# Kernel tuning notes

Measured on AMD Instinct MI355X. Metric: run time of the kernel, lower is better.

The kernel has to match this reference:

```python
import jax, jax.numpy as jnp
import numpy as np

C0, C1, C2 = 2000, 10000, 50000  # class cutoffs
D = 1024                          # input_size (hidden dim)
OUT_HEAD = C0 + 2                 # head output: shortlist + 2 cluster logits


def setup_inputs() -> dict:
    key = jax.random.key(0)
    ks = jax.random.split(key, 7)
    s = lambda fan_in: 1.0 / np.sqrt(fan_in)
    x = jax.random.normal(ks[0], (4096, D), dtype=jnp.float32)
    Wh = jax.random.normal(ks[1], (OUT_HEAD, D), dtype=jnp.float32) * s(D)
    bh = jnp.zeros((OUT_HEAD,), dtype=jnp.float32)
    # tail 0: D -> D//4**0 -> (C1-C0)
    W0a = jax.random.normal(ks[2], (D, D), dtype=jnp.float32) * s(D)
    W0b = jax.random.normal(ks[3], (C1 - C0, D), dtype=jnp.float32) * s(D)
    # tail 1: D -> D//4**1 -> (C2-C1)
    W1a = jax.random.normal(ks[4], (D // 4, D), dtype=jnp.float32) * s(D)
    W1b = jax.random.normal(ks[5], (C2 - C1, D // 4), dtype=jnp.float32) * s(D // 4)
    return {"x": x, "Wh": Wh, "bh": bh, "W0a": W0a, "W0b": W0b, "W1a": W1a, "W1b": W1b}


def reference(x, Wh, bh, W0a, W0b, W1a, W1b):
    # head: [B, OUT_HEAD]; log-softmax over shortlist + cluster logits
    lsm_head = jax.nn.log_softmax(x @ Wh.T + bh, axis=-1)
    # tail clusters: capacity-reduction linear, projection, log-softmax within cluster
    lsm_t0 = jax.nn.log_softmax((x @ W0a.T) @ W0b.T, axis=-1)  # [B, C1-C0]
    lsm_t1 = jax.nn.log_softmax((x @ W1a.T) @ W1b.T, axis=-1)  # [B, C2-C1]
    # flat log-probs: cluster log-prob broadcast-added to within-cluster log-probs
    prob = jnp.concatenate([
        lsm_head[:, :C0],
        lsm_head[:, C0:C0 + 1] + lsm_t0,
        lsm_head[:, C0 + 1:C0 + 2] + lsm_t1,
    ], axis=1)  # [B, C2]
    return prob
```

## Files before the change

kernel.cpp:

```cpp
#include <hip/hip_runtime.h>
#include <hip/hip_bf16.h>
#include <math.h>

#define CC0 2000
#define CC1 10000
#define CC2 50000
#define DH  1024
#define BATCH 4096
#define OUT_HEAD (CC0 + 2)

#define N0_P 8192
#define N1_P 40192
#define NH_P 2048

typedef __attribute__((ext_vector_type(4))) float  f32x4;
typedef __attribute__((ext_vector_type(8))) __bf16 bf16x8;
typedef __attribute__((ext_vector_type(8))) short  s16x8;

__device__ __forceinline__ void gload_lds16(const void* g, void* l) {
    __builtin_amdgcn_global_load_lds(
        (const __attribute__((address_space(1))) void*)g,
        (__attribute__((address_space(3))) void*)l, 16, 0, 0);
}

__global__ __launch_bounds__(256) void convert_all_kernel(
    const float4* __restrict__ s0, ushort4* __restrict__ d0, int n0s, int n0d,
    const float4* __restrict__ s1, ushort4* __restrict__ d1, int n1s, int n1d,
    const float4* __restrict__ s2, ushort4* __restrict__ d2, int n2s, int n2d,
    const float4* __restrict__ s3, ushort4* __restrict__ d3, int n3s, int n3d,
    const float4* __restrict__ s4, ushort4* __restrict__ d4, int n4s, int n4d,
    const float4* __restrict__ s5, ushort4* __restrict__ d5, int n5s, int n5d,
    float* __restrict__ rs0, float* __restrict__ rs1)
{
    if (blockIdx.y == 6) {
        int i = blockIdx.x * blockDim.x + threadIdx.x;
        if (i < BATCH) { rs0[i] = 0.f; rs1[i] = 0.f; }
        return;
    }
    const float4* src; ushort4* dst; int ns, nd;
    switch (blockIdx.y) {
        case 0: src = s0; dst = d0; ns = n0s; nd = n0d; break;
        case 1: src = s1; dst = d1; ns = n1s; nd = n1d; break;
        case 2: src = s2; dst = d2; ns = n2s; nd = n2d; break;
        case 3: src = s3; dst = d3; ns = n3s; nd = n3d; break;
        case 4: src = s4; dst = d4; ns = n4s; nd = n4d; break;
        default: src = s5; dst = d5; ns = n5s; nd = n5d; break;
    }
    int i = blockIdx.x * blockDim.x + threadIdx.x;
    const int stride = gridDim.x * blockDim.x;
    for (; i < nd; i += stride) {
        ushort4 o = {0, 0, 0, 0};
        if (i < ns) {
            float4 v = src[i];
            o.x = __builtin_bit_cast(unsigned short, (__bf16)v.x);
            o.y = __builtin_bit_cast(unsigned short, (__bf16)v.y);
            o.z = __builtin_bit_cast(unsigned short, (__bf16)v.z);
            o.w = __builtin_bit_cast(unsigned short, (__bf16)v.w);
        }
        dst[i] = o;
    }
}

__global__ __launch_bounds__(256) void gemm128x3_kernel(
    const ushort* __restrict__ x_bf,
    const ushort* __restrict__ W0a_bf, ushort* __restrict__ h0,
    const ushort* __restrict__ W1a_bf, ushort* __restrict__ h1,
    const ushort* __restrict__ Wh_bf,  float*  __restrict__ headL)
{
    __shared__ ushort As[128 * 64];
    __shared__ ushort Bs[128 * 64];

    const int gb = blockIdx.x;
    const ushort* B; void* C;
    int N, ldC, wmode, nbx, lin;
    const int K = DH;
    if (gb < 256)      { B = W0a_bf; C = h0;    N = DH;       ldC = DH;       wmode = 1; nbx = 8;  lin = gb; }
    else if (gb < 320) { B = W1a_bf; C = h1;    N = 256;      ldC = 256;      wmode = 1; nbx = 2;  lin = gb - 256; }
    else               { B = Wh_bf;  C = headL; N = OUT_HEAD; ldC = OUT_HEAD; wmode = 2; nbx = 16; lin = gb - 320; }

    const int nwg = nbx * 32;
    const int q = nwg >> 3;
    int bid = (lin & 7) * q + (lin >> 3);
    const int bx = bid % nbx;
    const int by = bid / nbx;

    const int t = threadIdx.x;
    const int lane = t & 63;
    const int w = t >> 6;
    const int wr = w >> 1, wc = w & 1;
    const int lr = lane & 15;
    const int lg = lane >> 4;
    const int bm = by * 128;
    const int bn = bx * 128;
    const int lrow = lane >> 3;
    const int lcol = (lane & 7) * 8;

    f32x4 acc[4][4] = {};

    for (int k0 = 0; k0 < K; k0 += 64) {
        #pragma unroll
        for (int i = 0; i < 4; ++i) {
            const int seg = w * 4 + i;
            const int row = seg * 8 + lrow;
            gload_lds16(x_bf + (size_t)(bm + row) * K + k0 + lcol, &As[seg * 512]);
            gload_lds16(B + (size_t)(bn + row) * K + k0 + lcol, &Bs[seg * 512]);
        }
        __syncthreads();
        #pragma unroll
        for (int ks = 0; ks < 2; ++ks) {
            s16x8 af[4], bfr[4];
            #pragma unroll
            for (int m = 0; m < 4; ++m)
                af[m] = *(const s16x8*)&As[(wr * 64 + m * 16 + lr) * 64 + ks * 32 + lg * 8];
            #pragma unroll
            for (int n = 0; n < 4; ++n)
                bfr[n] = *(const s16x8*)&Bs[(wc * 64 + n * 16 + lr) * 64 + ks * 32 + lg * 8];
            #pragma unroll
            for (int m = 0; m < 4; ++m)
                #pragma unroll
                for (int n = 0; n < 4; ++n)
                    acc[m][n] = __builtin_amdgcn_mfma_f32_16x16x32_bf16(
                        __builtin_bit_cast(bf16x8, af[m]),
                        __builtin_bit_cast(bf16x8, bfr[n]), acc[m][n], 0, 0, 0);
        }
        __syncthreads();
    }

    #pragma unroll
    for (int m = 0; m < 4; ++m)
        #pragma unroll
        for (int r = 0; r < 4; ++r) {
            const int row = bm + wr * 64 + m * 16 + lg * 4 + r;
            #pragma unroll
            for (int n = 0; n < 4; ++n) {
                const int col = bn + wc * 64 + n * 16 + lr;
                float v = acc[m][n][r];
                if (col < N) {
                    if (wmode == 1)
                        ((ushort*)C)[(size_t)row * ldC + col] =
                            __builtin_bit_cast(unsigned short, (__bf16)v);
                    else
                        ((float*)C)[(size_t)row * ldC + col] = v;
                }
            }
        }
}

__global__ __launch_bounds__(512, 1) void tails256_kernel(
    const ushort* __restrict__ h0, const ushort* __restrict__ W0b,
    ushort* __restrict__ L0, float* __restrict__ rs0,
    const ushort* __restrict__ h1, const ushort* __restrict__ W1b,
    ushort* __restrict__ L1, float* __restrict__ rs1)
{
    __shared__ ushort lds[2][2][256 * 64];

    const int gb = blockIdx.x;
    const ushort *A, *B; ushort* C; float* rsum;
    int K, N, nbx, ldC, lin;
    if (gb < 512) { A = h0; B = W0b; C = L0; rsum = rs0; K = DH;  N = CC1 - CC0; nbx = N0_P / 256; ldC = N0_P; lin = gb; }
    else          { A = h1; B = W1b; C = L1; rsum = rs1; K = 256; N = CC2 - CC1; nbx = N1_P / 256; ldC = N1_P; lin = gb - 512; }

    const int nwg = nbx * 16;
    const int q8 = nwg >> 3;
    int bid = (lin & 7) * q8 + (lin >> 3);
    const int by = bid % 16;
    const int bx = bid / 16;
    const int bm = by * 256, bn = bx * 256;

    const int t = threadIdx.x;
    const int lane = t & 63;
    const int w = t >> 6;
    const int wr = w >> 2;
    const int wc = w & 3;
    const int lr = lane & 15;
    const int lg = lane >> 4;
    const int xr = (lr & 7) << 4;
    const int c0 = w * 64 + lane;

    f32x4 acc[8][4] = {};
    const int nkt = K / 64;

    auto stage_tile = [&](int ktile, int buf) {
        const int k0 = ktile * 64;
        #pragma unroll
        for (int h = 0; h < 4; ++h) {
            const int r0 = (h >> 1) * 128;
            const int mat = h & 1;
            const ushort* gbase = mat ? B : A;
            const int brow = mat ? bn : bm;
            #pragma unroll
            for (int i = 0; i < 2; ++i) {
                const int c = i * 512 + c0;
                const int rl = c >> 3;
                const int cc = (c & 7) ^ (rl & 7);
                gload_lds16(gbase + (size_t)(brow + r0 + rl) * K + k0 + cc * 8,
                            (char*)&lds[buf][mat][0] + r0 * 128 + (i * 512 + w * 64) * 16);
            }
        }
    };

    stage_tile(0, 0);
    asm volatile("s_waitcnt vmcnt(0)");
    __builtin_amdgcn_s_barrier();
    asm volatile("" ::: "memory");

    for (int tk = 0; tk < nkt; ++tk) {
        const int cur = tk & 1;
        if (tk + 1 < nkt) stage_tile(tk + 1, cur ^ 1);
        const char* baseA = (const char*)&lds[cur][0][0];
        const char* baseB = (const char*)&lds[cur][1][0];

        s16x8 bfr[4][2];
        #pragma unroll
        for (int n_ = 0; n_ < 4; ++n_) {
            const int row = wc * 64 + n_ * 16 + lr;
            #pragma unroll
            for (int ks = 0; ks < 2; ++ks)
                bfr[n_][ks] = *(const s16x8*)(baseB + (row * 128 + ((ks * 64 + lg * 16) ^ xr)));
        }
        #pragma unroll
        for (int mh = 0; mh < 2; ++mh) {
            s16x8 af[4][2];
            #pragma unroll
            for (int m_ = 0; m_ < 4; ++m_) {
                const int row = wr * 128 + (mh * 4 + m_) * 16 + lr;
                #pragma unroll
                for (int ks = 0; ks < 2; ++ks)
                    af[m_][ks] = *(const s16x8*)(baseA + (row * 128 + ((ks * 64 + lg * 16) ^ xr)));
            }
            __builtin_amdgcn_s_setprio(1);
            #pragma unroll
            for (int m_ = 0; m_ < 4; ++m_)
                #pragma unroll
                for (int n_ = 0; n_ < 4; ++n_)
                    #pragma unroll
                    for (int ks = 0; ks < 2; ++ks)
                        acc[mh * 4 + m_][n_] = __builtin_amdgcn_mfma_f32_16x16x32_bf16(
                            __builtin_bit_cast(bf16x8, af[m_][ks]),
                            __builtin_bit_cast(bf16x8, bfr[n_][ks]),
                            acc[mh * 4 + m_][n_], 0, 0, 0);
            __builtin_amdgcn_s_setprio(0);
        }
        asm volatile("s_waitcnt vmcnt(0)" ::: "memory");
        __builtin_amdgcn_s_barrier();
        asm volatile("" ::: "memory");
    }

    #pragma unroll
    for (int m = 0; m < 8; ++m) {
        #pragma unroll
        for (int r = 0; r < 4; ++r) {
            const int row = bm + wr * 128 + m * 16 + lg * 4 + r;
            float psum = 0.f;
            #pragma unroll
            for (int n = 0; n < 4; ++n) {
                const int col = bn + wc * 64 + n * 16 + lr;
                float v = acc[m][n][r];
                if (col < N) {
                    C[(size_t)row * ldC + col] =
                        __builtin_bit_cast(unsigned short, (__bf16)v);
                    psum += __expf(v);
                }
            }
            #pragma unroll
            for (int mm = 1; mm < 16; mm <<= 1) psum += __shfl_xor(psum, mm, 64);
            if (lr == 0) atomicAdd(&rsum[row], psum);
        }
    }
}

__global__ __launch_bounds__(256) void head_lsm_kernel(
    const float* __restrict__ HL, const float* __restrict__ bh,
    float* __restrict__ out, float* __restrict__ s01)
{
    const int row = blockIdx.x;
    const float* L = HL + (size_t)row * OUT_HEAD;
    const int t = threadIdx.x;
    __shared__ float red[4];

    float m = -1e30f;
    for (int i = t; i < OUT_HEAD; i += 256) m = fmaxf(m, L[i] + bh[i]);
    #pragma unroll
    for (int s = 1; s < 64; s <<= 1) m = fmaxf(m, __shfl_xor(m, s, 64));
    if ((t & 63) == 0) red[t >> 6] = m;
    __syncthreads();
    m = fmaxf(fmaxf(red[0], red[1]), fmaxf(red[2], red[3]));

    float sum = 0.f;
    for (int i = t; i < OUT_HEAD; i += 256) sum += __expf(L[i] + bh[i] - m);
    #pragma unroll
    for (int s = 1; s < 64; s <<= 1) sum += __shfl_xor(sum, s, 64);
    __syncthreads();
    if ((t & 63) == 0) red[t >> 6] = sum;
    __syncthreads();
    const float lse = m + logf(red[0] + red[1] + red[2] + red[3]);

    float* orow = out + (size_t)row * CC2;
    for (int i = t; i < CC0; i += 256) orow[i] = L[i] + bh[i] - lse;
    if (t == 0) {
        s01[2 * row + 0] = L[CC0 + 0] + bh[CC0 + 0] - lse;
        s01[2 * row + 1] = L[CC0 + 1] + bh[CC0 + 1] - lse;
    }
}

__global__ __launch_bounds__(256) void prep_add_kernel(
    const float* __restrict__ s01, const float* __restrict__ rs0,
    const float* __restrict__ rs1, float* __restrict__ add0,
    float* __restrict__ add1, int n)
{
    int i = blockIdx.x * blockDim.x + threadIdx.x;
    if (i < n) {
        add0[i] = s01[2 * i + 0] - logf(rs0[i]);
        add1[i] = s01[2 * i + 1] - logf(rs1[i]);
    }
}

__global__ __launch_bounds__(256) void finalize_all_kernel(
    const ushort* __restrict__ L0, const ushort* __restrict__ L1,
    const float* __restrict__ add0, const float* __restrict__ add1,
    float* __restrict__ out)
{
    const int row = blockIdx.y;
    const int c = blockIdx.x * blockDim.x + threadIdx.x;
    const ushort* src; float* dst; float add;
    if (c < 1000) {
        src = L0 + (size_t)row * N0_P + c * 8;
        dst = out + (size_t)row * CC2 + CC0 + c * 8;
        add = add0[row];
    } else if (c < 6000) {
        const int c1 = c - 1000;
        src = L1 + (size_t)row * N1_P + c1 * 8;
        dst = out + (size_t)row * CC2 + CC1 + c1 * 8;
        add = add1[row];
    } else return;
    s16x8 v = *(const s16x8*)src;
    float4 o0, o1;
    o0.x = __builtin_bit_cast(float, (unsigned)(unsigned short)v[0] << 16) + add;
    o0.y = __builtin_bit_cast(float, (unsigned)(unsigned short)v[1] << 16) + add;
    o0.z = __builtin_bit_cast(float, (unsigned)(unsigned short)v[2] << 16) + add;
    o0.w = __builtin_bit_cast(float, (unsigned)(unsigned short)v[3] << 16) + add;
    o1.x = __builtin_bit_cast(float, (unsigned)(unsigned short)v[4] << 16) + add;
    o1.y = __builtin_bit_cast(float, (unsigned)(unsigned short)v[5] << 16) + add;
    o1.z = __builtin_bit_cast(float, (unsigned)(unsigned short)v[6] << 16) + add;
    o1.w = __builtin_bit_cast(float, (unsigned)(unsigned short)v[7] << 16) + add;
    *(float4*)dst = o0;
    *(float4*)(dst + 4) = o1;
}

extern "C" void kernel_launch(void* const* d_in, const int* in_sizes, int n_in,
                              void* d_out, int out_size, void* d_ws, size_t ws_size,
                              hipStream_t stream) {
    const float* x   = (const float*)d_in[0];
    const float* Wh  = (const float*)d_in[1];
    const float* bh  = (const float*)d_in[2];
    const float* W0a = (const float*)d_in[3];
    const float* W0b = (const float*)d_in[4];
    const float* W1a = (const float*)d_in[5];
    const float* W1b = (const float*)d_in[6];
    float* out = (float*)d_out;
    char*  ws  = (char*)d_ws;

    size_t off = 0;
    auto alloc = [&](size_t bytes) { size_t o = off; off += (bytes + 255) & ~(size_t)255; return o; };
    ushort* x_bf   = (ushort*)(ws + alloc((size_t)BATCH * DH * 2));
    ushort* Wh_bf  = (ushort*)(ws + alloc((size_t)NH_P * DH * 2));
    ushort* W0a_bf = (ushort*)(ws + alloc((size_t)DH * DH * 2));
    ushort* W0b_bf = (ushort*)(ws + alloc((size_t)N0_P * DH * 2));
    ushort* W1a_bf = (ushort*)(ws + alloc((size_t)256 * DH * 2));
    ushort* W1b_bf = (ushort*)(ws + alloc((size_t)N1_P * 256 * 2));
    ushort* h0_bf  = (ushort*)(ws + alloc((size_t)BATCH * DH * 2));
    ushort* h1_bf  = (ushort*)(ws + alloc((size_t)BATCH * 256 * 2));
    float*  headL  = (float*)(ws + alloc((size_t)BATCH * OUT_HEAD * 4));
    float*  s01    = (float*)(ws + alloc((size_t)BATCH * 2 * 4));
    float*  rs0    = (float*)(ws + alloc((size_t)BATCH * 4));
    float*  rs1    = (float*)(ws + alloc((size_t)BATCH * 4));
    float*  add0   = (float*)(ws + alloc((size_t)BATCH * 4));
    float*  add1   = (float*)(ws + alloc((size_t)BATCH * 4));
    ushort* L0     = (ushort*)(ws + alloc((size_t)BATCH * N0_P * 2));
    ushort* L1     = (ushort*)(ws + alloc((size_t)BATCH * N1_P * 2));

    convert_all_kernel<<<dim3(1280, 7), 256, 0, stream>>>(
        (const float4*)x,   (ushort4*)x_bf,   BATCH * DH / 4,        BATCH * DH / 4,
        (const float4*)Wh,  (ushort4*)Wh_bf,  OUT_HEAD * DH / 4,     NH_P * DH / 4,
        (const float4*)W0a, (ushort4*)W0a_bf, DH * DH / 4,           DH * DH / 4,
        (const float4*)W0b, (ushort4*)W0b_bf, (CC1 - CC0) * DH / 4,  N0_P * DH / 4,
        (const float4*)W1a, (ushort4*)W1a_bf, 256 * DH / 4,          256 * DH / 4,
        (const float4*)W1b, (ushort4*)W1b_bf, (CC2 - CC1) * 256 / 4, N1_P * 256 / 4,
        rs0, rs1);

    gemm128x3_kernel<<<832, 256, 0, stream>>>(
        x_bf, W0a_bf, h0_bf, W1a_bf, h1_bf, Wh_bf, headL);

    head_lsm_kernel<<<BATCH, 256, 0, stream>>>(headL, bh, out, s01);

    tails256_kernel<<<512 + (N1_P / 256) * 16, 512, 0, stream>>>(
        h0_bf, W0b_bf, L0, rs0, h1_bf, W1b_bf, L1, rs1);

    prep_add_kernel<<<(BATCH + 255) / 256, 256, 0, stream>>>(s01, rs0, rs1, add0, add1, BATCH);

    finalize_all_kernel<<<dim3(24, BATCH), 256, 0, stream>>>(L0, L1, add0, add1, out);
}
```

Measured before the change: 616.9 us.

## Overlap weight conversion with GEMMs and pipeline tail GEMMs with finalize by row halves

The W0b/W1b fp32-to-bf16 conversion moves into extra blocks of the first GEMM kernel, so it can overlap with the head and projection GEMMs. The tail GEMMs are split into two launches over halves of the batch rows. The finalize step for the first half (log-sum-exp add and bf16-to-fp32 expansion) is appended as extra blocks of the second-half GEMM launch, and the separate prep_add kernel is folded into finalize. The goal is to hide memory-bound conversion and finalize work behind compute-bound GEMMs and to cut launch count. In exchange, each tail GEMM launch has fewer blocks and finalize blocks compete with GEMM blocks for CUs.

```diff
diff --git a/kernel.cpp b/kernel.cpp
--- a/kernel.cpp
+++ b/kernel.cpp
@@ -12,6 +12,10 @@
 #define N0_P 8192
 #define N1_P 40192
 #define NH_P 2048
+#define GROUP_ROWS 2048
+#define T1_NBX (N1_P / 256)
+#define T0_NBX (N0_P / 256)
+#define GEMM_BLOCKS (8 * T0_NBX + 8 * T1_NBX)
 
 typedef __attribute__((ext_vector_type(4))) float  f32x4;
 typedef __attribute__((ext_vector_type(8))) __bf16 bf16x8;
@@ -23,32 +27,10 @@
         (__attribute__((address_space(3))) void*)l, 16, 0, 0);
 }
 
-__global__ __launch_bounds__(256) void convert_all_kernel(
-    const float4* __restrict__ s0, ushort4* __restrict__ d0, int n0s, int n0d,
-    const float4* __restrict__ s1, ushort4* __restrict__ d1, int n1s, int n1d,
-    const float4* __restrict__ s2, ushort4* __restrict__ d2, int n2s, int n2d,
-    const float4* __restrict__ s3, ushort4* __restrict__ d3, int n3s, int n3d,
-    const float4* __restrict__ s4, ushort4* __restrict__ d4, int n4s, int n4d,
-    const float4* __restrict__ s5, ushort4* __restrict__ d5, int n5s, int n5d,
-    float* __restrict__ rs0, float* __restrict__ rs1)
-{
-    if (blockIdx.y == 6) {
-        int i = blockIdx.x * blockDim.x + threadIdx.x;
-        if (i < BATCH) { rs0[i] = 0.f; rs1[i] = 0.f; }
-        return;
-    }
-    const float4* src; ushort4* dst; int ns, nd;
-    switch (blockIdx.y) {
-        case 0: src = s0; dst = d0; ns = n0s; nd = n0d; break;
-        case 1: src = s1; dst = d1; ns = n1s; nd = n1d; break;
-        case 2: src = s2; dst = d2; ns = n2s; nd = n2d; break;
-        case 3: src = s3; dst = d3; ns = n3s; nd = n3d; break;
-        case 4: src = s4; dst = d4; ns = n4s; nd = n4d; break;
-        default: src = s5; dst = d5; ns = n5s; nd = n5d; break;
-    }
-    int i = blockIdx.x * blockDim.x + threadIdx.x;
-    const int stride = gridDim.x * blockDim.x;
-    for (; i < nd; i += stride) {
+__device__ __forceinline__ void cvt_range(const float4* __restrict__ src,
+                                          ushort4* __restrict__ dst,
+                                          int ns, int nd, int start, int stride) {
+    for (int i = start; i < nd; i += stride) {
         ushort4 o = {0, 0, 0, 0};
         if (i < ns) {
             float4 v = src[i];
@@ -61,16 +43,48 @@
     }
 }
 
-__global__ __launch_bounds__(256) void gemm128x3_kernel(
+__global__ __launch_bounds__(256) void convert_small_kernel(
+    const float4* __restrict__ x,   ushort4* __restrict__ x_bf,
+    const float4* __restrict__ Wh,  ushort4* __restrict__ Wh_bf,
+    const float4* __restrict__ W0a, ushort4* __restrict__ W0a_bf,
+    const float4* __restrict__ W1a, ushort4* __restrict__ W1a_bf,
+    float* __restrict__ rs0, float* __restrict__ rs1)
+{
+    const int start = blockIdx.x * blockDim.x + threadIdx.x;
+    const int stride = gridDim.x * blockDim.x;
+    switch (blockIdx.y) {
+        case 0: cvt_range(x,   x_bf,   BATCH * DH / 4,    BATCH * DH / 4, start, stride); break;
+        case 1: cvt_range(Wh,  Wh_bf,  OUT_HEAD * DH / 4, NH_P * DH / 4,  start, stride); break;
+        case 2: cvt_range(W0a, W0a_bf, DH * DH / 4,       DH * DH / 4,    start, stride); break;
+        case 3: cvt_range(W1a, W1a_bf, 256 * DH / 4,      256 * DH / 4,   start, stride); break;
+        default:
+            if (start < BATCH) { rs0[start] = 0.f; rs1[start] = 0.f; }
+            break;
+    }
+}
+
+__global__ __launch_bounds__(256) void gemm128x3_conv_kernel(
     const ushort* __restrict__ x_bf,
     const ushort* __restrict__ W0a_bf, ushort* __restrict__ h0,
     const ushort* __restrict__ W1a_bf, ushort* __restrict__ h1,
-    const ushort* __restrict__ Wh_bf,  float*  __restrict__ headL)
+    const ushort* __restrict__ Wh_bf,  float*  __restrict__ headL,
+    const float4* __restrict__ W0b,  ushort4* __restrict__ W0b_bf,
+    const float4* __restrict__ W1b,  ushort4* __restrict__ W1b_bf)
 {
     __shared__ ushort As[128 * 64];
     __shared__ ushort Bs[128 * 64];
 
     const int gb = blockIdx.x;
+    if (gb >= 832) {
+        if (gb < 1344)
+            cvt_range(W0b, W0b_bf, (CC1 - CC0) * DH / 4, N0_P * DH / 4,
+                      (gb - 832) * 256 + threadIdx.x, 512 * 256);
+        else
+            cvt_range(W1b, W1b_bf, (CC2 - CC1) * 256 / 4, N1_P * 256 / 4,
+                      (gb - 1344) * 256 + threadIdx.x, 512 * 256);
+        return;
+    }
+
     const ushort* B; void* C;
     int N, ldC, wmode, nbx, lin;
     const int K = DH;
@@ -146,26 +160,90 @@
         }
 }
 
-__global__ __launch_bounds__(512, 1) void tails256_kernel(
+__global__ __launch_bounds__(256) void head_lsm_kernel(
+    const float* __restrict__ HL, const float* __restrict__ bh,
+    float* __restrict__ out, float* __restrict__ s01)
+{
+    const int row = blockIdx.x;
+    const float* L = HL + (size_t)row * OUT_HEAD;
+    const int t = threadIdx.x;
+    __shared__ float red[4];
+
+    float m = -1e30f;
+    for (int i = t; i < OUT_HEAD; i += 256) m = fmaxf(m, L[i] + bh[i]);
+    #pragma unroll
+    for (int s = 1; s < 64; s <<= 1) m = fmaxf(m, __shfl_xor(m, s, 64));
+    if ((t & 63) == 0) red[t >> 6] = m;
+    __syncthreads();
+    m = fmaxf(fmaxf(red[0], red[1]), fmaxf(red[2], red[3]));
+
+    float sum = 0.f;
+    for (int i = t; i < OUT_HEAD; i += 256) sum += __expf(L[i] + bh[i] - m);
+    #pragma unroll
+    for (int s = 1; s < 64; s <<= 1) sum += __shfl_xor(sum, s, 64);
+    __syncthreads();
+    if ((t & 63) == 0) red[t >> 6] = sum;
+    __syncthreads();
+    const float lse = m + logf(red[0] + red[1] + red[2] + red[3]);
+
+    float* orow = out + (size_t)row * CC2;
+    for (int i = t; i < CC0; i += 256) orow[i] = L[i] + bh[i] - lse;
+    if (t == 0) {
+        s01[2 * row + 0] = L[CC0 + 0] + bh[CC0 + 0] - lse;
+        s01[2 * row + 1] = L[CC0 + 1] + bh[CC0 + 1] - lse;
+    }
+}
+
+__global__ __launch_bounds__(512, 1) void tails_pipe_kernel(
     const ushort* __restrict__ h0, const ushort* __restrict__ W0b,
     ushort* __restrict__ L0, float* __restrict__ rs0,
     const ushort* __restrict__ h1, const ushort* __restrict__ W1b,
-    ushort* __restrict__ L1, float* __restrict__ rs1)
+    ushort* __restrict__ L1, float* __restrict__ rs1,
+    const float* __restrict__ s01, float* __restrict__ out,
+    int ggrp, int ngemm, int fin_base)
 {
     __shared__ ushort lds[2][2][256 * 64];
 
     const int gb = blockIdx.x;
+    if (gb >= ngemm) {
+        const int row = fin_base + (gb - ngemm);
+        const float a0 = s01[2 * row + 0] - logf(rs0[row]);
+        const float a1 = s01[2 * row + 1] - logf(rs1[row]);
+        const ushort* r0 = L0 + (size_t)row * N0_P;
+        const ushort* r1 = L1 + (size_t)row * N1_P;
+        float* o = out + (size_t)row * CC2;
+        for (int c = threadIdx.x; c < 6000; c += 512) {
+            const bool t0 = c < 1000;
+            const ushort* src = t0 ? r0 + c * 8 : r1 + (c - 1000) * 8;
+            float* dst = t0 ? o + CC0 + c * 8 : o + CC1 + (c - 1000) * 8;
+            const float add = t0 ? a0 : a1;
+            s16x8 v = *(const s16x8*)src;
+            float4 o0, o1;
+            o0.x = __builtin_bit_cast(float, (unsigned)(unsigned short)v[0] << 16) + add;
+            o0.y = __builtin_bit_cast(float, (unsigned)(unsigned short)v[1] << 16) + add;
+            o0.z = __builtin_bit_cast(float, (unsigned)(unsigned short)v[2] << 16) + add;
+            o0.w = __builtin_bit_cast(float, (unsigned)(unsigned short)v[3] << 16) + add;
+            o1.x = __builtin_bit_cast(float, (unsigned)(unsigned short)v[4] << 16) + add;
+            o1.y = __builtin_bit_cast(float, (unsigned)(unsigned short)v[5] << 16) + add;
+            o1.z = __builtin_bit_cast(float, (unsigned)(unsigned short)v[6] << 16) + add;
+            o1.w = __builtin_bit_cast(float, (unsigned)(unsigned short)v[7] << 16) + add;
+            *(float4*)dst = o0;
+            *(float4*)(dst + 4) = o1;
+        }
+        return;
+    }
+
     const ushort *A, *B; ushort* C; float* rsum;
     int K, N, nbx, ldC, lin;
-    if (gb < 512) { A = h0; B = W0b; C = L0; rsum = rs0; K = DH;  N = CC1 - CC0; nbx = N0_P / 256; ldC = N0_P; lin = gb; }
-    else          { A = h1; B = W1b; C = L1; rsum = rs1; K = 256; N = CC2 - CC1; nbx = N1_P / 256; ldC = N1_P; lin = gb - 512; }
-
-    const int nwg = nbx * 16;
+    if (gb < 8 * T0_NBX) { A = h0; B = W0b; C = L0; rsum = rs0; K = DH;  N = CC1 - CC0; nbx = T0_NBX; ldC = N0_P; lin = gb; }
+    else                 { A = h1; B = W1b; C = L1; rsum = rs1; K = 256; N = CC2 - CC1; nbx = T1_NBX; ldC = N1_P; lin = gb - 8 * T0_NBX; }
+
+    const int nwg = nbx * 8;
     const int q8 = nwg >> 3;
     int bid = (lin & 7) * q8 + (lin >> 3);
-    const int by = bid % 16;
-    const int bx = bid / 16;
-    const int bm = by * 256, bn = bx * 256;
+    const int by = bid % 8;
+    const int bx = bid / 8;
+    const int bm = ggrp * GROUP_ROWS + by * 256, bn = bx * 256;
 
     const int t = threadIdx.x;
     const int lane = t & 63;
@@ -267,84 +345,6 @@
             if (lr == 0) atomicAdd(&rsum[row], psum);
         }
     }
-}
-
-__global__ __launch_bounds__(256) void head_lsm_kernel(
-    const float* __restrict__ HL, const float* __restrict__ bh,
-    float* __restrict__ out, float* __restrict__ s01)
-{
-    const int row = blockIdx.x;
-    const float* L = HL + (size_t)row * OUT_HEAD;
-    const int t = threadIdx.x;
-    __shared__ float red[4];
-
-    float m = -1e30f;
-    for (int i = t; i < OUT_HEAD; i += 256) m = fmaxf(m, L[i] + bh[i]);
-    #pragma unroll
-    for (int s = 1; s < 64; s <<= 1) m = fmaxf(m, __shfl_xor(m, s, 64));
-    if ((t & 63) == 0) red[t >> 6] = m;
-    __syncthreads();
-    m = fmaxf(fmaxf(red[0], red[1]), fmaxf(red[2], red[3]));
-
-    float sum = 0.f;
-    for (int i = t; i < OUT_HEAD; i += 256) sum += __expf(L[i] + bh[i] - m);
-    #pragma unroll
-    for (int s = 1; s < 64; s <<= 1) sum += __shfl_xor(sum, s, 64);
-    __syncthreads();
-    if ((t & 63) == 0) red[t >> 6] = sum;
-    __syncthreads();
-    const float lse = m + logf(red[0] + red[1] + red[2] + red[3]);
-
-    float* orow = out + (size_t)row * CC2;
-    for (int i = t; i < CC0; i += 256) orow[i] = L[i] + bh[i] - lse;
-    if (t == 0) {
-        s01[2 * row + 0] = L[CC0 + 0] + bh[CC0 + 0] - lse;
-        s01[2 * row + 1] = L[CC0 + 1] + bh[CC0 + 1] - lse;
-    }
-}
-
-__global__ __launch_bounds__(256) void prep_add_kernel(
-    const float* __restrict__ s01, const float* __restrict__ rs0,
-    const float* __restrict__ rs1, float* __restrict__ add0,
-    float* __restrict__ add1, int n)
-{
-    int i = blockIdx.x * blockDim.x + threadIdx.x;
-    if (i < n) {
-        add0[i] = s01[2 * i + 0] - logf(rs0[i]);
-        add1[i] = s01[2 * i + 1] - logf(rs1[i]);
-    }
-}
-
-__global__ __launch_bounds__(256) void finalize_all_kernel(
-    const ushort* __restrict__ L0, const ushort* __restrict__ L1,
-    const float* __restrict__ add0, const float* __restrict__ add1,
-    float* __restrict__ out)
-{
-    const int row = blockIdx.y;
-    const int c = blockIdx.x * blockDim.x + threadIdx.x;
-    const ushort* src; float* dst; float add;
-    if (c < 1000) {
-        src = L0 + (size_t)row * N0_P + c * 8;
-        dst = out + (size_t)row * CC2 + CC0 + c * 8;
-        add = add0[row];
-    } else if (c < 6000) {
-        const int c1 = c - 1000;
-        src = L1 + (size_t)row * N1_P + c1 * 8;
-        dst = out + (size_t)row * CC2 + CC1 + c1 * 8;
-        add = add1[row];
-    } else return;
-    s16x8 v = *(const s16x8*)src;
-    float4 o0, o1;
-    o0.x = __builtin_bit_cast(float, (unsigned)(unsigned short)v[0] << 16) + add;
-    o0.y = __builtin_bit_cast(float, (unsigned)(unsigned short)v[1] << 16) + add;
-    o0.z = __builtin_bit_cast(float, (unsigned)(unsigned short)v[2] << 16) + add;
-    o0.w = __builtin_bit_cast(float, (unsigned)(unsigned short)v[3] << 16) + add;
-    o1.x = __builtin_bit_cast(float, (unsigned)(unsigned short)v[4] << 16) + add;
-    o1.y = __builtin_bit_cast(float, (unsigned)(unsigned short)v[5] << 16) + add;
-    o1.z = __builtin_bit_cast(float, (unsigned)(unsigned short)v[6] << 16) + add;
-    o1.w = __builtin_bit_cast(float, (unsigned)(unsigned short)v[7] << 16) + add;
-    *(float4*)dst = o0;
-    *(float4*)(dst + 4) = o1;
 }
 
 extern "C" void kernel_launch(void* const* d_in, const int* in_sizes, int n_in,
@@ -374,29 +374,30 @@
     float*  s01    = (float*)(ws + alloc((size_t)BATCH * 2 * 4));
     float*  rs0    = (float*)(ws + alloc((size_t)BATCH * 4));
     float*  rs1    = (float*)(ws + alloc((size_t)BATCH * 4));
-    float*  add0   = (float*)(ws + alloc((size_t)BATCH * 4));
-    float*  add1   = (float*)(ws + alloc((size_t)BATCH * 4));
     ushort* L0     = (ushort*)(ws + alloc((size_t)BATCH * N0_P * 2));
     ushort* L1     = (ushort*)(ws + alloc((size_t)BATCH * N1_P * 2));
 
-    convert_all_kernel<<<dim3(1280, 7), 256, 0, stream>>>(
-        (const float4*)x,   (ushort4*)x_bf,   BATCH * DH / 4,        BATCH * DH / 4,
-        (const float4*)Wh,  (ushort4*)Wh_bf,  OUT_HEAD * DH / 4,     NH_P * DH / 4,
-        (const float4*)W0a, (ushort4*)W0a_bf, DH * DH / 4,           DH * DH / 4,
-        (const float4*)W0b, (ushort4*)W0b_bf, (CC1 - CC0) * DH / 4,  N0_P * DH / 4,
-        (const float4*)W1a, (ushort4*)W1a_bf, 256 * DH / 4,          256 * DH / 4,
-        (const float4*)W1b, (ushort4*)W1b_bf, (CC2 - CC1) * 256 / 4, N1_P * 256 / 4,
+    convert_small_kernel<<<dim3(1024, 5), 256, 0, stream>>>(
+        (const float4*)x,   (ushort4*)x_bf,
+        (const float4*)Wh,  (ushort4*)Wh_bf,
+        (const float4*)W0a, (ushort4*)W0a_bf,
+        (const float4*)W1a, (ushort4*)W1a_bf,
         rs0, rs1);
 
-    gemm128x3_kernel<<<832, 256, 0, stream>>>(
-        x_bf, W0a_bf, h0_bf, W1a_bf, h1_bf, Wh_bf, headL);
+    gemm128x3_conv_kernel<<<1856, 256, 0, stream>>>(
+        x_bf, W0a_bf, h0_bf, W1a_bf, h1_bf, Wh_bf, headL,
+        (const float4*)W0b, (ushort4*)W0b_bf,
+        (const float4*)W1b, (ushort4*)W1b_bf);
 
     head_lsm_kernel<<<BATCH, 256, 0, stream>>>(headL, bh, out, s01);
 
-    tails256_kernel<<<512 + (N1_P / 256) * 16, 512, 0, stream>>>(
-        h0_bf, W0b_bf, L0, rs0, h1_bf, W1b_bf, L1, rs1);
-
-    prep_add_kernel<<<(BATCH + 255) / 256, 256, 0, stream>>>(s01, rs0, rs1, add0, add1, BATCH);
-
-    finalize_all_kernel<<<dim3(24, BATCH), 256, 0, stream>>>(L0, L1, add0, add1, out);
-}
+    tails_pipe_kernel<<<GEMM_BLOCKS, 512, 0, stream>>>(
+        h0_bf, W0b_bf, L0, rs0, h1_bf, W1b_bf, L1, rs1, s01, out,
+        0, GEMM_BLOCKS, 0);
+    tails_pipe_kernel<<<GEMM_BLOCKS + GROUP_ROWS, 512, 0, stream>>>(
+        h0_bf, W0b_bf, L0, rs0, h1_bf, W1b_bf, L1, rs1, s01, out,
+        1, GEMM_BLOCKS, 0);
+    tails_pipe_kernel<<<GROUP_ROWS, 512, 0, stream>>>(
+        h0_bf, W0b_bf, L0, rs0, h1_bf, W1b_bf, L1, rs1, s01, out,
+        0, 0, GROUP_ROWS);
+}
```

Result: slower. 677.1 us (+9.7%).

## Split GEMM K-tile prefetch into quarter chunks with finer-grained waits and barriers

Applied to the files above, without the earlier changes.

Restructures the double-buffered GEMM main loop so each 64-wide K tile is staged in four chunks: the A and B row halves are remapped so that each chunk covers one (mh, nh) quadrant of the next tile. Each quadrant's MFMAs run after a partial vmcnt wait and a barrier, which interleaves global-to-LDS loads with compute instead of issuing all loads up front and waiting at the end of the iteration. This adds four barriers per K iteration instead of one and reloads A fragments twice per tile (once per nh), which raises LDS read traffic.

```diff
diff --git a/kernel.cpp b/kernel.cpp
--- a/kernel.cpp
+++ b/kernel.cpp
@@ -180,47 +180,55 @@
     f32x4 acc[8][4] = {};
     const int nkt = K / 64;
 
-    auto stage_tile = [&](int ktile, int buf) {
+    auto stage_chunk = [&](int ktile, int buf, int p) {
         const int k0 = ktile * 64;
-        #pragma unroll
-        for (int h = 0; h < 4; ++h) {
-            const int r0 = (h >> 1) * 128;
-            const int mat = h & 1;
-            const ushort* gbase = mat ? B : A;
-            const int brow = mat ? bn : bm;
-            #pragma unroll
-            for (int i = 0; i < 2; ++i) {
-                const int c = i * 512 + c0;
-                const int rl = c >> 3;
-                const int cc = (c & 7) ^ (rl & 7);
-                gload_lds16(gbase + (size_t)(brow + r0 + rl) * K + k0 + cc * 8,
-                            (char*)&lds[buf][mat][0] + r0 * 128 + (i * 512 + w * 64) * 16);
-            }
+        const int mat = (p == 1 || p == 2) ? 1 : 0;
+        const int j = p >> 1;
+        const ushort* gbase = mat ? B : A;
+        const int brow = mat ? bn : bm;
+        #pragma unroll
+        for (int i = 0; i < 2; ++i) {
+            const int v = i * 512 + c0;
+            const int vrow = v >> 3;
+            int ar;
+            if (mat == 0) ar = ((vrow >> 6) << 7) + (j << 6) + (vrow & 63);
+            else          ar = ((vrow >> 5) << 6) + (j << 5) + (vrow & 31);
+            const int cc = (v & 7) ^ (ar & 7);
+            const int v0 = (i * 512 + w * 64) >> 3;
+            int ar0;
+            if (mat == 0) ar0 = ((v0 >> 6) << 7) + (j << 6) + (v0 & 63);
+            else          ar0 = ((v0 >> 5) << 6) + (j << 5) + (v0 & 31);
+            gload_lds16(gbase + (size_t)(brow + ar) * K + k0 + cc * 8,
+                        (char*)&lds[buf][mat][0] + ar0 * 128);
         }
     };
 
-    stage_tile(0, 0);
-    asm volatile("s_waitcnt vmcnt(0)");
+    #pragma unroll
+    for (int p = 0; p < 4; ++p) stage_chunk(0, 0, p);
+    asm volatile("s_waitcnt vmcnt(0)" ::: "memory");
     __builtin_amdgcn_s_barrier();
     asm volatile("" ::: "memory");
 
     for (int tk = 0; tk < nkt; ++tk) {
         const int cur = tk & 1;
-        if (tk + 1 < nkt) stage_tile(tk + 1, cur ^ 1);
         const char* baseA = (const char*)&lds[cur][0][0];
         const char* baseB = (const char*)&lds[cur][1][0];
-
-        s16x8 bfr[4][2];
-        #pragma unroll
-        for (int n_ = 0; n_ < 4; ++n_) {
-            const int row = wc * 64 + n_ * 16 + lr;
-            #pragma unroll
-            for (int ks = 0; ks < 2; ++ks)
-                bfr[n_][ks] = *(const s16x8*)(baseB + (row * 128 + ((ks * 64 + lg * 16) ^ xr)));
-        }
-        #pragma unroll
-        for (int mh = 0; mh < 2; ++mh) {
-            s16x8 af[4][2];
+        const bool more = (tk + 1 < nkt);
+        #pragma unroll
+        for (int p = 0; p < 4; ++p) {
+            const int mh = p >> 1, nh = p & 1;
+            if (more) {
+                stage_chunk(tk + 1, cur ^ 1, p);
+                asm volatile("s_waitcnt vmcnt(6)" ::: "memory");
+            } else {
+                if (p == 0)      asm volatile("s_waitcnt vmcnt(4)" ::: "memory");
+                else if (p == 1) asm volatile("s_waitcnt vmcnt(2)" ::: "memory");
+                else if (p == 2) asm volatile("s_waitcnt vmcnt(0)" ::: "memory");
+            }
+            __builtin_amdgcn_s_barrier();
+            asm volatile("" ::: "memory");
+
+            s16x8 af[4][2], bq[2][2];
             #pragma unroll
             for (int m_ = 0; m_ < 4; ++m_) {
                 const int row = wr * 128 + (mh * 4 + m_) * 16 + lr;
@@ -228,22 +236,26 @@
                 for (int ks = 0; ks < 2; ++ks)
                     af[m_][ks] = *(const s16x8*)(baseA + (row * 128 + ((ks * 64 + lg * 16) ^ xr)));
             }
+            #pragma unroll
+            for (int n_ = 0; n_ < 2; ++n_) {
+                const int row = wc * 64 + (nh * 2 + n_) * 16 + lr;
+                #pragma unroll
+                for (int ks = 0; ks < 2; ++ks)
+                    bq[n_][ks] = *(const s16x8*)(baseB + (row * 128 + ((ks * 64 + lg * 16) ^ xr)));
+            }
             __builtin_amdgcn_s_setprio(1);
             #pragma unroll
             for (int m_ = 0; m_ < 4; ++m_)
                 #pragma unroll
-                for (int n_ = 0; n_ < 4; ++n_)
+                for (int n_ = 0; n_ < 2; ++n_)
                     #pragma unroll
                     for (int ks = 0; ks < 2; ++ks)
-                        acc[mh * 4 + m_][n_] = __builtin_amdgcn_mfma_f32_16x16x32_bf16(
+                        acc[mh * 4 + m_][nh * 2 + n_] = __builtin_amdgcn_mfma_f32_16x16x32_bf16(
                             __builtin_bit_cast(bf16x8, af[m_][ks]),
-                            __builtin_bit_cast(bf16x8, bfr[n_][ks]),
-                            acc[mh * 4 + m_][n_], 0, 0, 0);
+                            __builtin_bit_cast(bf16x8, bq[n_][ks]),
+                            acc[mh * 4 + m_][nh * 2 + n_], 0, 0, 0);
             __builtin_amdgcn_s_setprio(0);
         }
-        asm volatile("s_waitcnt vmcnt(0)" ::: "memory");
-        __builtin_amdgcn_s_barrier();
-        asm volatile("" ::: "memory");
     }
 
     #pragma unroll
```

Measured after the change: 606.1 us. Within noise of the previous version (-1.8%).
